# Kernel tuning notes

Measured on AMD Instinct MI355X. Metric: run time of the kernel, lower is better.

The kernel has to match this reference:

```python
import jax, jax.numpy as jnp
import numpy as np

LN_EPS = 1e-10


def _log_g(x):
    # log of g(x) where g(x) = x + 0.5 for x >= 0 else sigmoid(x)
    return jnp.where(x >= 0, jnp.log(jax.nn.relu(x) + 0.5), -jax.nn.softplus(-x))


def setup_inputs() -> dict:
    key = jax.random.key(0)
    k1, k2 = jax.random.split(key)
    B, T, D, H = 8, 4096, 512, 512
    x = jax.random.normal(k1, (B, T, D), dtype=jnp.float32)
    ln_gamma = jnp.ones((D,), dtype=jnp.float32)
    ln_beta = jnp.zeros((D,), dtype=jnp.float32)
    W_gh = jax.random.normal(k2, (D, 2 * H), dtype=jnp.float32) * 0.02
    return {"x": x, "ln_gamma": ln_gamma, "ln_beta": ln_beta, "W_gh": W_gh}


def reference(x, ln_gamma, ln_beta, W_gh):
    # LayerNorm over last dim
    mu = jnp.mean(x, axis=-1, keepdims=True)
    var = jnp.mean(jnp.square(x - mu), axis=-1, keepdims=True)
    xn = (x - mu) * jax.lax.rsqrt(var + LN_EPS) * ln_gamma + ln_beta

    # minGRU projection: gate logits k and candidate pre-activation
    gh = jnp.einsum('btd,dh->bth', xn, W_gh)  # [B, T, 2H]
    H = W_gh.shape[1] // 2
    k_gate, h_pre = gh[..., :H], gh[..., H:]

    # log-space parallel scan (Heinsen): h_t = (1-z_t) h_{t-1} + z_t g(h_pre_t)
    log_z = -jax.nn.softplus(-k_gate)        # log sigmoid(k)
    log_coeffs = -jax.nn.softplus(k_gate)    # log(1 - sigmoid(k))
    log_values = log_z + _log_g(h_pre)

    a_star = jnp.cumsum(log_coeffs, axis=1)
    log_h = a_star + jax.lax.cumlogsumexp(log_values - a_star, axis=1)
    h = jnp.exp(log_h)  # [B, T, H]

    # residual (res_proj is Identity since input_size == hidden_size)
    out = h + x
    hidden = h[:, -1]  # last hidden state [B, H]
    return out, hidden
```

## Files before the change

kernel.cpp:

```cpp
#include <hip/hip_runtime.h>
#include <stdint.h>

#define NB 8
#define NT 4096
#define ND 512
#define NH 512
#define NN 1024
#define NM (NB * NT)
#define NK 512
#define NCH 128
#define CTS 32

typedef __bf16 bf16x8 __attribute__((ext_vector_type(8)));
typedef float floatx4 __attribute__((ext_vector_type(4)));
typedef unsigned int uint_g __attribute__((address_space(1)));
typedef unsigned int uint_l __attribute__((address_space(3)));

__device__ __forceinline__ float bf2f(unsigned short u) {
    union { unsigned int i; float f; } v; v.i = ((unsigned int)u) << 16; return v.f;
}
__device__ __forceinline__ unsigned short f2bf(float f) {
    union { float f; unsigned int i; } v; v.f = f;
    return (unsigned short)((v.i + 0x7FFFu + ((v.i >> 16) & 1u)) >> 16);
}

__device__ __forceinline__ void load_lds16(const void* g, void* l) {
    __builtin_amdgcn_global_load_lds((const uint_g*)g, (uint_l*)l, 16, 0, 0);
}

__global__ __launch_bounds__(256) void prep_kernel(const float* __restrict__ x,
                                                   const float* __restrict__ gamma,
                                                   const float* __restrict__ beta,
                                                   const float* __restrict__ W,
                                                   unsigned short* __restrict__ xn,
                                                   unsigned short* __restrict__ Wt) {
    if (blockIdx.x < 512) {
        __shared__ float tile[32][33];
        int bid = blockIdx.x;
        int n0 = (bid & 31) * 32;
        int k0 = (bid >> 5) * 32;
        int tx = threadIdx.x & 31, ty = threadIdx.x >> 5;
#pragma unroll
        for (int j = 0; j < 4; ++j)
            tile[ty + j * 8][tx] = W[(size_t)(k0 + ty + j * 8) * NN + n0 + tx];
        __syncthreads();
#pragma unroll
        for (int j = 0; j < 4; ++j)
            Wt[(size_t)(n0 + ty + j * 8) * NK + k0 + tx] = f2bf(tile[tx][ty + j * 8]);
        return;
    }
    int wid = threadIdx.x >> 6, lane = threadIdx.x & 63;
    size_t row = (size_t)(blockIdx.x - 512) * 4 + wid;
    const float4* xr = (const float4*)(x + row * ND);
    float4 v0 = xr[lane];
    float4 v1 = xr[lane + 64];
    float s  = (v0.x + v0.y) + (v0.z + v0.w) + (v1.x + v1.y) + (v1.z + v1.w);
    float sq = v0.x * v0.x + v0.y * v0.y + v0.z * v0.z + v0.w * v0.w
             + v1.x * v1.x + v1.y * v1.y + v1.z * v1.z + v1.w * v1.w;
#pragma unroll
    for (int off = 32; off > 0; off >>= 1) {
        s  += __shfl_xor(s,  off, 64);
        sq += __shfl_xor(sq, off, 64);
    }
    float mu   = s * (1.0f / ND);
    float var  = sq * (1.0f / ND) - mu * mu;
    float rstd = rsqrtf(var + 1e-10f);
    const float4* gr = (const float4*)gamma;
    const float4* br = (const float4*)beta;
    float4 g0 = gr[lane], g1 = gr[lane + 64];
    float4 b0 = br[lane], b1 = br[lane + 64];
    ushort4 o0, o1;
    o0.x = f2bf((v0.x - mu) * rstd * g0.x + b0.x);
    o0.y = f2bf((v0.y - mu) * rstd * g0.y + b0.y);
    o0.z = f2bf((v0.z - mu) * rstd * g0.z + b0.z);
    o0.w = f2bf((v0.w - mu) * rstd * g0.w + b0.w);
    o1.x = f2bf((v1.x - mu) * rstd * g1.x + b1.x);
    o1.y = f2bf((v1.y - mu) * rstd * g1.y + b1.y);
    o1.z = f2bf((v1.z - mu) * rstd * g1.z + b1.z);
    o1.w = f2bf((v1.w - mu) * rstd * g1.w + b1.w);
    ushort4* xo = (ushort4*)(xn + row * ND);
    xo[lane]      = o0;
    xo[lane + 64] = o1;
}

__global__ __launch_bounds__(256) void gemm_kernel(const unsigned short* __restrict__ A,
                                                   const unsigned short* __restrict__ Bt,
                                                   unsigned short* __restrict__ C) {
    __shared__ __align__(16) unsigned short As[128 * 64];
    __shared__ __align__(16) unsigned short Bs[128 * 64];
    int tid  = threadIdx.x;
    int lane = tid & 63;
    int wid  = tid >> 6;
    int wm = wid & 1, wn = wid >> 1;
    int bx = blockIdx.x;
    int mt = bx & 255;
    int nt = bx >> 8;
    const int Rm = mt * 128, Rn = nt * 128;

    int rloc = lane >> 3;
    int cl   = lane & 7;
    int cg   = cl ^ rloc;

    int frow = lane & 15;
    int quad = lane >> 4;
    int fx   = lane & 7;

    floatx4 acc[4][4];
#pragma unroll
    for (int i = 0; i < 4; ++i)
#pragma unroll
        for (int j = 0; j < 4; ++j)
            acc[i][j] = (floatx4){0.f, 0.f, 0.f, 0.f};

#pragma unroll 1
    for (int kt = 0; kt < NK / 64; ++kt) {
        int k0 = kt * 64;
        __syncthreads();
#pragma unroll
        for (int s = 0; s < 4; ++s) {
            int g  = wid * 4 + s;
            int ml = g * 8 + rloc;
            load_lds16(A + (size_t)(Rm + ml) * NK + k0 + cg * 8, As + g * 512);
        }
#pragma unroll
        for (int s = 0; s < 4; ++s) {
            int g  = wid * 4 + s;
            int nl = g * 8 + rloc;
            load_lds16(Bt + (size_t)(Rn + nl) * NK + k0 + cg * 8, Bs + g * 512);
        }
        __syncthreads();
#pragma unroll
        for (int ks = 0; ks < 2; ++ks) {
            int ch = (ks * 4 + quad) ^ fx;
            bf16x8 af[4], bfr[4];
#pragma unroll
            for (int mi = 0; mi < 4; ++mi) {
                int ml = wm * 64 + mi * 16 + frow;
                af[mi] = *(const bf16x8*)(As + ml * 64 + ch * 8);
            }
#pragma unroll
            for (int ni = 0; ni < 4; ++ni) {
                int nl = wn * 64 + ni * 16 + frow;
                bfr[ni] = *(const bf16x8*)(Bs + nl * 64 + ch * 8);
            }
#pragma unroll
            for (int mi = 0; mi < 4; ++mi)
#pragma unroll
                for (int ni = 0; ni < 4; ++ni)
                    acc[mi][ni] = __builtin_amdgcn_mfma_f32_16x16x32_bf16(
                        af[mi], bfr[ni], acc[mi][ni], 0, 0, 0);
        }
    }
#pragma unroll
    for (int mi = 0; mi < 4; ++mi)
#pragma unroll
        for (int ni = 0; ni < 4; ++ni)
#pragma unroll
            for (int r = 0; r < 4; ++r) {
                int row = Rm + wm * 64 + mi * 16 + quad * 4 + r;
                int col = Rn + wn * 64 + ni * 16 + frow;
                C[(size_t)row * NN + col] = f2bf(acc[mi][ni][r]);
            }
}

__device__ __forceinline__ void gate_av(unsigned short ku, unsigned short pu,
                                        float& a, float& v) {
    float k = bf2f(ku), p = bf2f(pu);
    float e = __expf(k);
    a = __builtin_amdgcn_rcpf(1.0f + e);
    float z = e * a;
    float gneg = __builtin_amdgcn_rcpf(1.0f + __expf(-p));
    float g = (p >= 0.0f) ? (p + 0.5f) : gneg;
    v = z * g;
}

__global__ __launch_bounds__(128) void scan1_kernel(const unsigned short* __restrict__ gh,
                                                    float* __restrict__ cA,
                                                    float* __restrict__ cV) {
    int b = blockIdx.x >> 7, c = blockIdx.x & 127;
    int h = threadIdx.x * 4;
    const unsigned short* base = gh + ((size_t)(b * NT + c * CTS)) * NN + h;
    float A0 = 1.f, A1 = 1.f, A2 = 1.f, A3 = 1.f;
    float V0 = 0.f, V1 = 0.f, V2 = 0.f, V3 = 0.f;
#pragma unroll 1
    for (int tb = 0; tb < CTS; tb += 8) {
        ushort4 kb[8], hb[8];
#pragma unroll
        for (int j = 0; j < 8; ++j) {
            const unsigned short* p = base + (size_t)(tb + j) * NN;
            kb[j] = *(const ushort4*)p;
            hb[j] = *(const ushort4*)(p + NH);
        }
#pragma unroll
        for (int j = 0; j < 8; ++j) {
            float a, v;
            gate_av(kb[j].x, hb[j].x, a, v); V0 = a * V0 + v; A0 *= a;
            gate_av(kb[j].y, hb[j].y, a, v); V1 = a * V1 + v; A1 *= a;
            gate_av(kb[j].z, hb[j].z, a, v); V2 = a * V2 + v; A2 *= a;
            gate_av(kb[j].w, hb[j].w, a, v); V3 = a * V3 + v; A3 *= a;
        }
    }
    size_t o = ((size_t)b * NH + h) * NCH + c;
    cA[o] = A0; cA[o + NCH] = A1; cA[o + 2 * NCH] = A2; cA[o + 3 * NCH] = A3;
    cV[o] = V0; cV[o + NCH] = V1; cV[o + 2 * NCH] = V2; cV[o + 3 * NCH] = V3;
}

__global__ __launch_bounds__(256) void scan2_kernel(const float* __restrict__ cA,
                                                    const float* __restrict__ cV,
                                                    float* __restrict__ hinit) {
    int w = blockIdx.x * 4 + (threadIdx.x >> 6);
    int lane = threadIdx.x & 63;
    int b = w >> 9, h = w & 511;
    const float2* a2p = (const float2*)(cA + ((size_t)b * NH + h) * NCH);
    const float2* v2p = (const float2*)(cV + ((size_t)b * NH + h) * NCH);
    float2 a2 = a2p[lane];
    float2 v2 = v2p[lane];
    float A = a2.y * a2.x;
    float V = a2.y * v2.x + v2.y;
#pragma unroll
    for (int off = 1; off < 64; off <<= 1) {
        float Ap = __shfl_up(A, off, 64);
        float Vp = __shfl_up(V, off, 64);
        if (lane >= off) { V = A * Vp + V; A = A * Ap; }
    }
    float excl = __shfl_up(V, 1, 64);
    if (lane == 0) excl = 0.f;
    float e0 = excl;
    float e1 = a2.x * e0 + v2.x;
    hinit[((size_t)b * NCH + 2 * lane) * NH + h]     = e0;
    hinit[((size_t)b * NCH + 2 * lane + 1) * NH + h] = e1;
}

__global__ __launch_bounds__(128) void scan3_kernel(const unsigned short* __restrict__ gh,
                                                    const float* __restrict__ hinit,
                                                    const float* __restrict__ x,
                                                    float* __restrict__ out,
                                                    float* __restrict__ hidden) {
    int b = blockIdx.x >> 7, c = blockIdx.x & 127;
    int h = threadIdx.x * 4;
    size_t row0 = (size_t)(b * NT + c * CTS);
    const unsigned short* base = gh + row0 * NN + h;
    const float* xb = x + row0 * ND + h;
    float* ob = out + row0 * ND + h;
    float4 hv = *(const float4*)(hinit + ((size_t)b * NCH + c) * NH + h);
#pragma unroll 1
    for (int tb = 0; tb < CTS; tb += 8) {
        ushort4 kb[8], hb[8];
        float4 xv[8];
#pragma unroll
        for (int j = 0; j < 8; ++j) {
            const unsigned short* p = base + (size_t)(tb + j) * NN;
            kb[j] = *(const ushort4*)p;
            hb[j] = *(const ushort4*)(p + NH);
            xv[j] = *(const float4*)(xb + (size_t)(tb + j) * ND);
        }
#pragma unroll
        for (int j = 0; j < 8; ++j) {
            float a, v;
            gate_av(kb[j].x, hb[j].x, a, v); hv.x = a * hv.x + v;
            gate_av(kb[j].y, hb[j].y, a, v); hv.y = a * hv.y + v;
            gate_av(kb[j].z, hb[j].z, a, v); hv.z = a * hv.z + v;
            gate_av(kb[j].w, hb[j].w, a, v); hv.w = a * hv.w + v;
            float4 ov;
            ov.x = hv.x + xv[j].x; ov.y = hv.y + xv[j].y;
            ov.z = hv.z + xv[j].z; ov.w = hv.w + xv[j].w;
            *(float4*)(ob + (size_t)(tb + j) * ND) = ov;
        }
    }
    if (c == NCH - 1)
        *(float4*)(hidden + (size_t)b * NH + h) = hv;
}

extern "C" void kernel_launch(void* const* d_in, const int* in_sizes, int n_in,
                              void* d_out, int out_size, void* d_ws, size_t ws_size,
                              hipStream_t stream) {
    const float* x     = (const float*)d_in[0];
    const float* gamma = (const float*)d_in[1];
    const float* beta  = (const float*)d_in[2];
    const float* W     = (const float*)d_in[3];

    float* out    = (float*)d_out;
    float* hidden = out + (size_t)NM * ND;

    char* ws = (char*)d_ws;
    unsigned short* Wt = (unsigned short*)ws;
    unsigned short* gh = (unsigned short*)(ws + (size_t)(1u << 20));
    float* cA    = (float*)(ws + (size_t)(1u << 20) + (size_t)NM * NN * 2);
    float* cV    = cA + (size_t)NB * NCH * NH;
    float* hinit = cV + (size_t)NB * NCH * NH;
    unsigned short* xn = (unsigned short*)d_out;

    prep_kernel<<<512 + NM / 4, 256, 0, stream>>>(x, gamma, beta, W, xn, Wt);
    gemm_kernel<<<2048, 256, 0, stream>>>(xn, Wt, gh);
    scan1_kernel<<<NB * NCH, 128, 0, stream>>>(gh, cA, cV);
    scan2_kernel<<<1024, 256, 0, stream>>>(cA, cV, hinit);
    scan3_kernel<<<NB * NCH, 128, 0, stream>>>(gh, hinit, x, out, hidden);
}
```

Measured before the change: 215.8 us.

## Fuse chunk-local scan into GEMM epilogue with interleaved gate/candidate columns

Result: slower. 556.5 us (+157.9%).

```diff
diff --git a/kernel.cpp b/kernel.cpp
--- a/kernel.cpp
+++ b/kernel.cpp
@@ -13,6 +13,7 @@
 
 typedef __bf16 bf16x8 __attribute__((ext_vector_type(8)));
 typedef float floatx4 __attribute__((ext_vector_type(4)));
+typedef unsigned short ushortx8 __attribute__((ext_vector_type(8)));
 typedef unsigned int uint_g __attribute__((address_space(1)));
 typedef unsigned int uint_l __attribute__((address_space(3)));
 
@@ -26,6 +27,17 @@
 
 __device__ __forceinline__ void load_lds16(const void* g, void* l) {
     __builtin_amdgcn_global_load_lds((const uint_g*)g, (uint_l*)l, 16, 0, 0);
+}
+
+__device__ __forceinline__ void gate_av(unsigned short ku, unsigned short pu,
+                                        float& a, float& v) {
+    float k = bf2f(ku), p = bf2f(pu);
+    float e = __expf(k);
+    a = __builtin_amdgcn_rcpf(1.0f + e);
+    float z = e * a;
+    float gneg = __builtin_amdgcn_rcpf(1.0f + __expf(-p));
+    float g = (p >= 0.0f) ? (p + 0.5f) : gneg;
+    v = z * g;
 }
 
 __global__ __launch_bounds__(256) void prep_kernel(const float* __restrict__ x,
@@ -45,8 +57,11 @@
             tile[ty + j * 8][tx] = W[(size_t)(k0 + ty + j * 8) * NN + n0 + tx];
         __syncthreads();
 #pragma unroll
-        for (int j = 0; j < 4; ++j)
-            Wt[(size_t)(n0 + ty + j * 8) * NK + k0 + tx] = f2bf(tile[tx][ty + j * 8]);
+        for (int j = 0; j < 4; ++j) {
+            int n = n0 + ty + j * 8;
+            int np = 2 * (n & 511) + (n >> 9);
+            Wt[(size_t)np * NK + k0 + tx] = f2bf(tile[tx][ty + j * 8]);
+        }
         return;
     }
     int wid = threadIdx.x >> 6, lane = threadIdx.x & 63;
@@ -85,7 +100,9 @@
 
 __global__ __launch_bounds__(256) void gemm_kernel(const unsigned short* __restrict__ A,
                                                    const unsigned short* __restrict__ Bt,
-                                                   unsigned short* __restrict__ C) {
+                                                   unsigned short* __restrict__ C,
+                                                   float* __restrict__ cA,
+                                                   float* __restrict__ cV) {
     __shared__ __align__(16) unsigned short As[128 * 64];
     __shared__ __align__(16) unsigned short Bs[128 * 64];
     int tid  = threadIdx.x;
@@ -161,48 +178,33 @@
                 int col = Rn + wn * 64 + ni * 16 + frow;
                 C[(size_t)row * NN + col] = f2bf(acc[mi][ni][r]);
             }
-}
-
-__device__ __forceinline__ void gate_av(unsigned short ku, unsigned short pu,
-                                        float& a, float& v) {
-    float k = bf2f(ku), p = bf2f(pu);
-    float e = __expf(k);
-    a = __builtin_amdgcn_rcpf(1.0f + e);
-    float z = e * a;
-    float gneg = __builtin_amdgcn_rcpf(1.0f + __expf(-p));
-    float g = (p >= 0.0f) ? (p + 0.5f) : gneg;
-    v = z * g;
-}
-
-__global__ __launch_bounds__(128) void scan1_kernel(const unsigned short* __restrict__ gh,
-                                                    float* __restrict__ cA,
-                                                    float* __restrict__ cV) {
-    int b = blockIdx.x >> 7, c = blockIdx.x & 127;
-    int h = threadIdx.x * 4;
-    const unsigned short* base = gh + ((size_t)(b * NT + c * CTS)) * NN + h;
-    float A0 = 1.f, A1 = 1.f, A2 = 1.f, A3 = 1.f;
-    float V0 = 0.f, V1 = 0.f, V2 = 0.f, V3 = 0.f;
+
+    __threadfence();
+    __syncthreads();
+    int chk = tid >> 6;
+    int hh  = tid & 63;
+    const unsigned short* cb = C + (size_t)(Rm + chk * 32) * NN + Rn + 2 * hh;
+    float Aagg = 1.f, Vagg = 0.f;
 #pragma unroll 1
     for (int tb = 0; tb < CTS; tb += 8) {
-        ushort4 kb[8], hb[8];
-#pragma unroll
-        for (int j = 0; j < 8; ++j) {
-            const unsigned short* p = base + (size_t)(tb + j) * NN;
-            kb[j] = *(const ushort4*)p;
-            hb[j] = *(const ushort4*)(p + NH);
-        }
+        ushort2 kp[8];
+#pragma unroll
+        for (int j = 0; j < 8; ++j)
+            kp[j] = *(const ushort2*)(cb + (size_t)(tb + j) * NN);
 #pragma unroll
         for (int j = 0; j < 8; ++j) {
             float a, v;
-            gate_av(kb[j].x, hb[j].x, a, v); V0 = a * V0 + v; A0 *= a;
-            gate_av(kb[j].y, hb[j].y, a, v); V1 = a * V1 + v; A1 *= a;
-            gate_av(kb[j].z, hb[j].z, a, v); V2 = a * V2 + v; A2 *= a;
-            gate_av(kb[j].w, hb[j].w, a, v); V3 = a * V3 + v; A3 *= a;
-        }
-    }
-    size_t o = ((size_t)b * NH + h) * NCH + c;
-    cA[o] = A0; cA[o + NCH] = A1; cA[o + 2 * NCH] = A2; cA[o + 3 * NCH] = A3;
-    cV[o] = V0; cV[o + NCH] = V1; cV[o + 2 * NCH] = V2; cV[o + 3 * NCH] = V3;
+            gate_av(kp[j].x, kp[j].y, a, v);
+            Vagg = a * Vagg + v;
+            Aagg *= a;
+        }
+    }
+    int b   = mt >> 5;
+    int cg2 = (mt & 31) * 4 + chk;
+    int hg  = nt * 64 + hh;
+    size_t o = ((size_t)b * NH + hg) * NCH + cg2;
+    cA[o] = Aagg;
+    cV[o] = Vagg;
 }
 
 __global__ __launch_bounds__(256) void scan2_kernel(const float* __restrict__ cA,
@@ -239,28 +241,26 @@
     int b = blockIdx.x >> 7, c = blockIdx.x & 127;
     int h = threadIdx.x * 4;
     size_t row0 = (size_t)(b * NT + c * CTS);
-    const unsigned short* base = gh + row0 * NN + h;
+    const unsigned short* base = gh + row0 * NN + 2 * h;
     const float* xb = x + row0 * ND + h;
     float* ob = out + row0 * ND + h;
     float4 hv = *(const float4*)(hinit + ((size_t)b * NCH + c) * NH + h);
 #pragma unroll 1
     for (int tb = 0; tb < CTS; tb += 8) {
-        ushort4 kb[8], hb[8];
+        ushortx8 kp[8];
         float4 xv[8];
 #pragma unroll
         for (int j = 0; j < 8; ++j) {
-            const unsigned short* p = base + (size_t)(tb + j) * NN;
-            kb[j] = *(const ushort4*)p;
-            hb[j] = *(const ushort4*)(p + NH);
+            kp[j] = *(const ushortx8*)(base + (size_t)(tb + j) * NN);
             xv[j] = *(const float4*)(xb + (size_t)(tb + j) * ND);
         }
 #pragma unroll
         for (int j = 0; j < 8; ++j) {
             float a, v;
-            gate_av(kb[j].x, hb[j].x, a, v); hv.x = a * hv.x + v;
-            gate_av(kb[j].y, hb[j].y, a, v); hv.y = a * hv.y + v;
-            gate_av(kb[j].z, hb[j].z, a, v); hv.z = a * hv.z + v;
-            gate_av(kb[j].w, hb[j].w, a, v); hv.w = a * hv.w + v;
+            gate_av(kp[j][0], kp[j][1], a, v); hv.x = a * hv.x + v;
+            gate_av(kp[j][2], kp[j][3], a, v); hv.y = a * hv.y + v;
+            gate_av(kp[j][4], kp[j][5], a, v); hv.z = a * hv.z + v;
+            gate_av(kp[j][6], kp[j][7], a, v); hv.w = a * hv.w + v;
             float4 ov;
             ov.x = hv.x + xv[j].x; ov.y = hv.y + xv[j].y;
             ov.z = hv.z + xv[j].z; ov.w = hv.w + xv[j].w;
@@ -291,8 +291,7 @@
     unsigned short* xn = (unsigned short*)d_out;
 
     prep_kernel<<<512 + NM / 4, 256, 0, stream>>>(x, gamma, beta, W, xn, Wt);
-    gemm_kernel<<<2048, 256, 0, stream>>>(xn, Wt, gh);
-    scan1_kernel<<<NB * NCH, 128, 0, stream>>>(gh, cA, cV);
+    gemm_kernel<<<2048, 256, 0, stream>>>(xn, Wt, gh, cA, cV);
     scan2_kernel<<<1024, 256, 0, stream>>>(cA, cV, hinit);
     scan3_kernel<<<NB * NCH, 128, 0, stream>>>(gh, hinit, x, out, hidden);
 }
```
